# Kernel tuning notes

Hardware: AMD Instinct MI355X
Metric: run time of the kernel (lower is better)

Reference implementation:

```python
import jax, jax.numpy as jnp
import numpy as np

N = 131072      # points (rays x samples chunk)
E = 8           # spatial sub-networks (centroids)
DIN = 90        # encoded pos+dir features fed to sub-NeRFs (xyz_real=True -> x[:, 3:])
H = 256         # sub-NeRF hidden width
DOUT = 4        # rgb + sigma
MARGIN = 2.0    # boundary_margin
EPS = 1e-8


def setup_inputs() -> dict:
    key = jax.random.key(0)
    k = jax.random.split(key, 5)
    x_xyz = jax.random.uniform(k[0], (N, 3), dtype=jnp.float32)          # routing coords in [0,1)^3
    x_feat = jax.random.normal(k[1], (N, DIN), dtype=jnp.float32)        # encoded features
    x = jnp.concatenate([x_xyz, x_feat], axis=1)                         # [N, 3+DIN]
    centroids = jax.random.uniform(k[2], (E, 3), dtype=jnp.float32)
    W1 = jax.random.normal(k[3], (E, DIN, H), dtype=jnp.float32) * 0.05
    b1 = jnp.zeros((E, H), dtype=jnp.float32)
    W2 = jax.random.normal(k[4], (E, H, DOUT), dtype=jnp.float32) * 0.05
    b2 = jnp.zeros((E, DOUT), dtype=jnp.float32)
    return {"x": x, "centroids": centroids, "W1": W1, "b1": b1, "W2": W2, "b2": b2}


def reference(x, centroids, W1, b1, W2, b2):
    # --- centroid routing (torch.cdist equivalent) ---
    xyz = x[:, :3]                                                       # [N,3]
    d2 = jnp.sum((xyz[:, None, :] - centroids[None, :, :]) ** 2, axis=-1)
    dist = jnp.sqrt(jnp.maximum(d2, 0.0))                                # [N,E]
    inv = 1.0 / (dist + EPS)
    min_d = jnp.min(dist, axis=1, keepdims=True)                         # [N,1]
    inv = jnp.where(dist > MARGIN * min_d, 0.0, inv)                     # zero far experts
    weights = inv / jnp.sum(inv, axis=-1, keepdims=True)                 # [N,E], rows sum to 1

    # --- per-expert sub-NeRF MLP, weighted combine ---
    # Dense-equivalent of masked gather + weighted scatter-add: experts whose
    # weight is exactly 0 contribute nothing, matching the torch masked path.
    feat = x[:, 3:]                                                      # xyz_real=True -> drop xyz
    h = jax.nn.relu(jnp.einsum('nd,edh->enh', feat, W1) + b1[:, None, :])  # [E,N,H]
    out_e = jnp.einsum('enh,eho->eno', h, W2) + b2[:, None, :]             # [E,N,DOUT]
    return jnp.einsum('eno,ne->no', out_e, weights)                        # [N,DOUT]
```

## Files before the change

### kernel.cpp

```cpp
#include <hip/hip_runtime.h>

#define NPTS 131072
#define NE 8
#define DIN 90
#define NH 256

typedef __attribute__((ext_vector_type(8))) short bf16x8;
typedef __attribute__((ext_vector_type(4))) float f32x4;
typedef __attribute__((ext_vector_type(2))) float f32x2;
typedef __attribute__((ext_vector_type(4))) unsigned int u32x4;
typedef __attribute__((ext_vector_type(2))) unsigned int u32x2;
typedef __attribute__((ext_vector_type(4), aligned(4))) float f32x4a;
typedef __attribute__((ext_vector_type(2), aligned(4))) float f32x2a;

__device__ __forceinline__ unsigned short f2bf(float f) {
  unsigned int u = __float_as_uint(f);
  u += 0x7fffu + ((u >> 16) & 1u);
  return (unsigned short)(u >> 16);
}

#if defined(__has_builtin) && __has_builtin(__builtin_amdgcn_cvt_pk_bf16_f32)
typedef __attribute__((ext_vector_type(2))) __bf16 bf16x2;
__device__ __forceinline__ unsigned int pkbf(float f0, float f1) {
  bf16x2 r = __builtin_amdgcn_cvt_pk_bf16_f32(f0, f1);
  return __builtin_bit_cast(unsigned int, r);
}
#else
__device__ __forceinline__ unsigned int pkbf(float f0, float f1) {
  unsigned int u0 = __float_as_uint(f0) + 0x7fffu;
  unsigned int u1 = __float_as_uint(f1) + 0x7fffu;
  return __builtin_amdgcn_perm(u1, u0, 0x07060302u);
}
#endif

__device__ __forceinline__ bf16x8 cvt8(f32x4 a, f32x4 b) {
  u32x4 r;
  r[0] = pkbf(a[0], a[1]);
  r[1] = pkbf(a[2], a[3]);
  r[2] = pkbf(b[0], b[1]);
  r[3] = pkbf(b[2], b[3]);
  return __builtin_bit_cast(bf16x8, r);
}

__global__ __launch_bounds__(256) void prep(const float* __restrict__ W1,
                                            const float* __restrict__ W2,
                                            unsigned short* __restrict__ W1T,
                                            unsigned short* __restrict__ W2T) {
  const int t = threadIdx.x;
  if (blockIdx.x < 32) {
    const int e = blockIdx.x >> 2;
    const int n0 = (blockIdx.x & 3) * 64;
    __shared__ unsigned int ld[64][49];
    const int nl = t & 63;
    const int kq = t >> 6;
#pragma unroll
    for (int j = 0; j < 12; ++j) {
      const int kp2 = kq + 4 * j;
      const int k0 = 2 * kp2, k1 = k0 + 1;
      unsigned int lo = 0, hi = 0;
      if (k0 < DIN) lo = f2bf(W1[((size_t)e * DIN + k0) * NH + n0 + nl]);
      if (k1 < DIN) hi = f2bf(W1[((size_t)e * DIN + k1) * NH + n0 + nl]);
      ld[nl][kp2] = lo | (hi << 16);
    }
    __syncthreads();
    unsigned int* dst = (unsigned int*)(W1T + (size_t)(e * NH + n0) * 96);
#pragma unroll
    for (int j = 0; j < 12; ++j) {
      const int u = t + 256 * j;
      dst[u] = ld[u / 48][u % 48];
    }
  } else {
    const int e = blockIdx.x - 32;
    unsigned int* dst = (unsigned int*)W2T + (size_t)e * 2048;
    const float* src = W2 + (size_t)e * 1024;
#pragma unroll
    for (int j = 0; j < 8; ++j) {
      const int u = t + 256 * j;
      const int o = u >> 7;
      const int kp = u & 127;
      unsigned int v = 0;
      if (o < 4) {
        unsigned int lo = f2bf(src[(2 * kp) * 4 + o]);
        unsigned int hi = f2bf(src[(2 * kp + 1) * 4 + o]);
        v = lo | (hi << 16);
      }
      dst[u] = v;
    }
  }
}

__global__ __launch_bounds__(256, 3) void meganerf_main(
    const float* __restrict__ x, const float* __restrict__ cent,
    const float* __restrict__ b1, const float* __restrict__ b2,
    const unsigned short* __restrict__ W1T, const unsigned short* __restrict__ W2T,
    float* __restrict__ out) {
  __shared__ unsigned short sH[4 * 2048];
  __shared__ float sW[NE][64];
  __shared__ float sB2[64][4];
  __shared__ float sB1[NE * NH];

  const int t    = threadIdx.x;
  const int lane = t & 63;
  const int wid  = t >> 6;
  const int l15  = lane & 15;
  const int l4   = lane >> 4;
  const int row0 = blockIdx.x * 64;
  const int gbase = wid * 2048;

#pragma unroll
  for (int j = 0; j < 2; ++j)
    *(f32x4*)&sB1[t * 4 + j * 1024] = *(const f32x4a*)&b1[t * 4 + j * 1024];

  bf16x8 bfr[4][3];
#pragma unroll
  for (int nf = 0; nf < 4; ++nf) {
    const float* gr = x + (size_t)(row0 + 16 * nf + l15) * 93 + 3;
    f32x4 v0, v1;
    v0 = *(const f32x4a*)(gr + 8 * l4);
    v1 = *(const f32x4a*)(gr + 8 * l4 + 4);
    bfr[nf][0] = cvt8(v0, v1);
    v0 = *(const f32x4a*)(gr + 32 + 8 * l4);
    v1 = *(const f32x4a*)(gr + 36 + 8 * l4);
    bfr[nf][1] = cvt8(v0, v1);
    if (l4 < 3) {
      v0 = *(const f32x4a*)(gr + 64 + 8 * l4);
      v1 = *(const f32x4a*)(gr + 68 + 8 * l4);
    } else {
      f32x2 tl = *(const f32x2a*)(gr + 88);
      v0[0] = tl[0]; v0[1] = tl[1]; v0[2] = 0.f; v0[3] = 0.f;
      v1[0] = 0.f; v1[1] = 0.f; v1[2] = 0.f; v1[3] = 0.f;
    }
    bfr[nf][2] = cvt8(v0, v1);
  }

  if (t < 64) {
    const float* gx = x + (size_t)(row0 + t) * 93;
    float px = gx[0], py = gx[1], pz = gx[2];
    float dist[NE], inv[NE];
    float mind = 3.4e38f;
#pragma unroll
    for (int e = 0; e < NE; ++e) {
      float dx = px - cent[e * 3 + 0];
      float dy = py - cent[e * 3 + 1];
      float dz = pz - cent[e * 3 + 2];
      float d2 = dx * dx + dy * dy + dz * dz;
      float d = sqrtf(fmaxf(d2, 0.f));
      dist[e] = d;
      inv[e] = 1.f / (d + 1e-8f);
      mind = fminf(mind, d);
    }
    float s = 0.f;
#pragma unroll
    for (int e = 0; e < NE; ++e) {
      if (dist[e] > 2.0f * mind) inv[e] = 0.f;
      s += inv[e];
    }
    float rs = 1.f / s;
    float bb[4] = {0.f, 0.f, 0.f, 0.f};
#pragma unroll
    for (int e = 0; e < NE; ++e) {
      float w = inv[e] * rs;
      sW[e][t] = w;
#pragma unroll
      for (int o = 0; o < 4; ++o) bb[o] += w * b2[e * 4 + o];
    }
#pragma unroll
    for (int o = 0; o < 4; ++o) sB2[t][o] = bb[o];
  }
  __syncthreads();

  bf16x8 w1buf[2][6];
  bf16x8 bwbuf[2];
  float wv[4];

  auto loadW1 = [&](int idx, int buf) {
    const int e = idx >> 1, c = idx & 1;
    const unsigned short* p =
        W1T + (size_t)(e * NH + 128 * c + 32 * wid + l15) * 96 + 8 * l4;
#pragma unroll
    for (int mf = 0; mf < 2; ++mf)
#pragma unroll
      for (int ks = 0; ks < 3; ++ks)
        w1buf[buf][mf * 3 + ks] = *(const bf16x8*)(p + mf * (16 * 96) + 32 * ks);
  };
  auto loadBW = [&](int idx, int buf) {
    const int e = idx >> 1, c = idx & 1;
    bwbuf[buf] = *(const bf16x8*)(W2T + (size_t)(e * 16 + l15) * NH +
                                  128 * c + 32 * wid + 8 * l4);
  };

  loadBW(0, 0);
  loadW1(0, 0);

  f32x4 facc[4] = {{0.f, 0.f, 0.f, 0.f}, {0.f, 0.f, 0.f, 0.f},
                   {0.f, 0.f, 0.f, 0.f}, {0.f, 0.f, 0.f, 0.f}};

#pragma unroll 2
  for (int i = 0; i < 16; ++i) {
    const int e = i >> 1, c = i & 1, cur = i & 1, nxt = cur ^ 1;
    const int colbase = 128 * c + 32 * wid;

    f32x4 b1v0 = *(const f32x4*)&sB1[e * NH + colbase + 4 * l4];
    f32x4 b1v1 = *(const f32x4*)&sB1[e * NH + colbase + 16 + 4 * l4];
    if (c == 0) {
#pragma unroll
      for (int nf = 0; nf < 4; ++nf) wv[nf] = sW[e][16 * nf + l15];
    }

    const int ip = (i + 1) & 15;
    loadBW(ip, nxt);
    loadW1(ip, nxt);

#pragma unroll
    for (int mf = 0; mf < 2; ++mf) {
      const f32x4 b1v = (mf == 0) ? b1v0 : b1v1;
      f32x4 acc[4];
      __builtin_amdgcn_s_setprio(1);
#pragma unroll
      for (int nf = 0; nf < 4; ++nf)
        acc[nf] = __builtin_amdgcn_mfma_f32_16x16x32_bf16(
            w1buf[cur][mf * 3 + 0], bfr[nf][0], b1v, 0, 0, 0);
#pragma unroll
      for (int ks = 1; ks < 3; ++ks)
#pragma unroll
        for (int nf = 0; nf < 4; ++nf)
          acc[nf] = __builtin_amdgcn_mfma_f32_16x16x32_bf16(
              w1buf[cur][mf * 3 + ks], bfr[nf][ks], acc[nf], 0, 0, 0);
      __builtin_amdgcn_s_setprio(0);

#pragma unroll
      for (int nf = 0; nf < 4; ++nf) {
        const float w = wv[nf];
        f32x4 a = acc[nf];
        f32x2 p0, p1;
        p0[0] = a[0]; p0[1] = a[1];
        p1[0] = a[2]; p1[1] = a[3];
        const f32x2 z = {0.f, 0.f};
        p0 = __builtin_elementwise_max(p0, z) * w;
        p1 = __builtin_elementwise_max(p1, z) * w;
        u32x2 pk;
        pk[0] = pkbf(p0[0], p0[1]);
        pk[1] = pkbf(p1[0], p1[1]);
        *(u32x2*)&sH[gbase + (nf * 64 + (l15 + 16 * (2 * mf + (l4 >> 1)))) * 8 +
                     4 * (l4 & 1)] = pk;
      }
    }

    __builtin_amdgcn_s_setprio(1);
#pragma unroll
    for (int rf = 0; rf < 4; ++rf) {
      bf16x8 ah = *(const bf16x8*)&sH[gbase + (rf * 64 + lane) * 8];
      facc[rf] = __builtin_amdgcn_mfma_f32_16x16x32_bf16(ah, bwbuf[cur], facc[rf], 0, 0, 0);
    }
    __builtin_amdgcn_s_setprio(0);
  }

  __syncthreads();
  float* sOutP = (float*)sH;
  if (l15 < 4) {
#pragma unroll
    for (int rf = 0; rf < 4; ++rf)
#pragma unroll
      for (int r = 0; r < 4; ++r)
        sOutP[(wid * 64 + 16 * rf + 4 * l4 + r) * 4 + l15] = facc[rf][r];
  }
  __syncthreads();
  {
    const int row = t >> 2, o = t & 3;
    float v = sB2[row][o] + sOutP[(0 * 64 + row) * 4 + o] + sOutP[(1 * 64 + row) * 4 + o] +
              sOutP[(2 * 64 + row) * 4 + o] + sOutP[(3 * 64 + row) * 4 + o];
    out[row0 * 4 + t] = v;
  }
}

extern "C" void kernel_launch(void* const* d_in, const int* in_sizes, int n_in,
                              void* d_out, int out_size, void* d_ws, size_t ws_size,
                              hipStream_t stream) {
  const float* x    = (const float*)d_in[0];
  const float* cent = (const float*)d_in[1];
  const float* W1   = (const float*)d_in[2];
  const float* b1   = (const float*)d_in[3];
  const float* W2   = (const float*)d_in[4];
  const float* b2   = (const float*)d_in[5];
  float* out = (float*)d_out;

  unsigned short* W1T = (unsigned short*)d_ws;
  unsigned short* W2T = W1T + NE * NH * 96;

  prep<<<40, 256, 0, stream>>>(W1, W2, W1T, W2T);
  meganerf_main<<<NPTS / 64, 256, 0, stream>>>(x, cent, b1, b2, W1T, W2T, out);
}
```

Measured before the change: 163.5 us.

## Stage features in LDS and cut register pressure to raise occupancy

The bf16 input features, previously held in registers by every wave (12 bf16x8 per lane), are now converted once and stored in shared memory, with each wave loading its own 16 rows. Each MFMA step reads them back from LDS. The W1 double buffer is trimmed so only the first half of the next tile is prefetched, and the second half plus the W2 fragment are loaded within the current step. Launch bounds move from 3 to 4 blocks per CU. The aim is more resident waves to hide latency, paid for with extra LDS reads per step and less prefetch distance on weights.

```diff
diff --git a/kernel.cpp b/kernel.cpp
--- a/kernel.cpp
+++ b/kernel.cpp
@@ -89,12 +89,110 @@
   }
 }
 
-__global__ __launch_bounds__(256, 3) void meganerf_main(
+#define UNRL _Pragma("unroll")
+
+#define FEAT(KS, NF) \
+  (*(const bf16x8*)&sFeat[(((KS)*4 + l4) * 64 + 16 * (NF) + l15) * 8])
+
+#define MF(W_, F_, C_) __builtin_amdgcn_mfma_f32_16x16x32_bf16(W_, F_, C_, 0, 0, 0)
+
+#define LOADW1MF0(E_, C_, D0, D1, D2)                                           \
+  do {                                                                          \
+    const unsigned short* _p =                                                  \
+        W1T + (size_t)((E_) * NH + 128 * (C_) + 32 * wid + l15) * 96 + 8 * l4;  \
+    D0 = *(const bf16x8*)(_p);                                                  \
+    D1 = *(const bf16x8*)(_p + 32);                                             \
+    D2 = *(const bf16x8*)(_p + 64);                                             \
+  } while (0)
+
+#define LOADW1MF1(E_, C_)                                                       \
+  do {                                                                          \
+    const unsigned short* _p = W1T +                                            \
+        (size_t)((E_) * NH + 128 * (C_) + 32 * wid + 16 + l15) * 96 + 8 * l4;   \
+    w1m1_0 = *(const bf16x8*)(_p);                                              \
+    w1m1_1 = *(const bf16x8*)(_p + 32);                                         \
+    w1m1_2 = *(const bf16x8*)(_p + 64);                                         \
+  } while (0)
+
+#define LOADBW(E_, C_)                                                          \
+  do {                                                                          \
+    bw = *(const bf16x8*)(W2T + (size_t)((E_) * 16 + l15) * NH + 128 * (C_) +   \
+                          32 * wid + 8 * l4);                                   \
+  } while (0)
+
+#define EPI(MF_)                                                                \
+  UNRL for (int nf = 0; nf < 4; ++nf) {                                         \
+    const float _w = wv[nf];                                                    \
+    f32x4 _a = acc[nf];                                                         \
+    f32x2 _p0, _p1;                                                             \
+    _p0[0] = _a[0]; _p0[1] = _a[1];                                             \
+    _p1[0] = _a[2]; _p1[1] = _a[3];                                             \
+    const f32x2 _z = {0.f, 0.f};                                                \
+    _p0 = __builtin_elementwise_max(_p0, _z) * _w;                              \
+    _p1 = __builtin_elementwise_max(_p1, _z) * _w;                              \
+    u32x2 _pk;                                                                  \
+    _pk[0] = pkbf(_p0[0], _p0[1]);                                              \
+    _pk[1] = pkbf(_p1[0], _p1[1]);                                              \
+    *(u32x2*)&sH[gbase + (nf * 64 + (l15 + 16 * (2 * (MF_) + (l4 >> 1)))) * 8 + \
+                 4 * (l4 & 1)] = _pk;                                           \
+  }
+
+#define STEPD(E_, C_, LDWV_, EN_, CN_, CM0, CM1, CM2, NM0, NM1, NM2)            \
+  do {                                                                          \
+    const int _cb = 128 * (C_) + 32 * wid;                                      \
+    f32x4 _b1v0 = *(const f32x4*)&sB1[(E_) * NH + _cb + 4 * l4];                \
+    f32x4 _b1v1 = *(const f32x4*)&sB1[(E_) * NH + _cb + 16 + 4 * l4];           \
+    if (LDWV_) {                                                                \
+      UNRL for (int nf = 0; nf < 4; ++nf) wv[nf] = sW[(E_)][16 * nf + l15];     \
+    }                                                                           \
+    LOADW1MF1(E_, C_);                                                          \
+    LOADBW(E_, C_);                                                             \
+    LOADW1MF0(EN_, CN_, NM0, NM1, NM2);                                         \
+    {                                                                           \
+      f32x4 acc[4];                                                             \
+      bf16x8 _f0, _f1, _f2, _f3;                                                \
+      __builtin_amdgcn_s_setprio(1);                                            \
+      _f0 = FEAT(0, 0); _f1 = FEAT(0, 1); _f2 = FEAT(0, 2); _f3 = FEAT(0, 3);   \
+      acc[0] = MF(CM0, _f0, _b1v0); acc[1] = MF(CM0, _f1, _b1v0);               \
+      acc[2] = MF(CM0, _f2, _b1v0); acc[3] = MF(CM0, _f3, _b1v0);               \
+      _f0 = FEAT(1, 0); _f1 = FEAT(1, 1); _f2 = FEAT(1, 2); _f3 = FEAT(1, 3);   \
+      acc[0] = MF(CM1, _f0, acc[0]); acc[1] = MF(CM1, _f1, acc[1]);             \
+      acc[2] = MF(CM1, _f2, acc[2]); acc[3] = MF(CM1, _f3, acc[3]);             \
+      _f0 = FEAT(2, 0); _f1 = FEAT(2, 1); _f2 = FEAT(2, 2); _f3 = FEAT(2, 3);   \
+      acc[0] = MF(CM2, _f0, acc[0]); acc[1] = MF(CM2, _f1, acc[1]);             \
+      acc[2] = MF(CM2, _f2, acc[2]); acc[3] = MF(CM2, _f3, acc[3]);             \
+      __builtin_amdgcn_s_setprio(0);                                            \
+      EPI(0)                                                                    \
+      asm volatile("" ::: "memory");     \
+      __builtin_amdgcn_s_setprio(1);                                            \
+      _f0 = FEAT(0, 0); _f1 = FEAT(0, 1); _f2 = FEAT(0, 2); _f3 = FEAT(0, 3);   \
+      acc[0] = MF(w1m1_0, _f0, _b1v1); acc[1] = MF(w1m1_0, _f1, _b1v1);         \
+      acc[2] = MF(w1m1_0, _f2, _b1v1); acc[3] = MF(w1m1_0, _f3, _b1v1);         \
+      _f0 = FEAT(1, 0); _f1 = FEAT(1, 1); _f2 = FEAT(1, 2); _f3 = FEAT(1, 3);   \
+      acc[0] = MF(w1m1_1, _f0, acc[0]); acc[1] = MF(w1m1_1, _f1, acc[1]);       \
+      acc[2] = MF(w1m1_1, _f2, acc[2]); acc[3] = MF(w1m1_1, _f3, acc[3]);       \
+      _f0 = FEAT(2, 0); _f1 = FEAT(2, 1); _f2 = FEAT(2, 2); _f3 = FEAT(2, 3);   \
+      acc[0] = MF(w1m1_2, _f0, acc[0]); acc[1] = MF(w1m1_2, _f1, acc[1]);       \
+      acc[2] = MF(w1m1_2, _f2, acc[2]); acc[3] = MF(w1m1_2, _f3, acc[3]);       \
+      __builtin_amdgcn_s_setprio(0);                                            \
+      EPI(1)                                                                    \
+    }                                                                           \
+    __builtin_amdgcn_s_setprio(1);                                              \
+    UNRL for (int rf = 0; rf < 4; ++rf) {                                       \
+      bf16x8 _ah = *(const bf16x8*)&sH[gbase + (rf * 64 + lane) * 8];           \
+      facc[rf] = __builtin_amdgcn_mfma_f32_16x16x32_bf16(_ah, bw, facc[rf],     \
+                                                         0, 0, 0);              \
+    }                                                                           \
+    __builtin_amdgcn_s_setprio(0);                                              \
+  } while (0)
+
+__global__ __launch_bounds__(256, 4) void meganerf_main2(
     const float* __restrict__ x, const float* __restrict__ cent,
     const float* __restrict__ b1, const float* __restrict__ b2,
     const unsigned short* __restrict__ W1T, const unsigned short* __restrict__ W2T,
     float* __restrict__ out) {
   __shared__ unsigned short sH[4 * 2048];
+  __shared__ unsigned short sFeat[12 * 512];
   __shared__ float sW[NE][64];
   __shared__ float sB2[64][4];
   __shared__ float sB1[NE * NH];
@@ -111,17 +209,15 @@
   for (int j = 0; j < 2; ++j)
     *(f32x4*)&sB1[t * 4 + j * 1024] = *(const f32x4a*)&b1[t * 4 + j * 1024];
 
-  bf16x8 bfr[4][3];
-#pragma unroll
-  for (int nf = 0; nf < 4; ++nf) {
-    const float* gr = x + (size_t)(row0 + 16 * nf + l15) * 93 + 3;
+  {
+    const float* gr = x + (size_t)(row0 + 16 * wid + l15) * 93 + 3;
     f32x4 v0, v1;
     v0 = *(const f32x4a*)(gr + 8 * l4);
     v1 = *(const f32x4a*)(gr + 8 * l4 + 4);
-    bfr[nf][0] = cvt8(v0, v1);
+    *(bf16x8*)&sFeat[((0 * 4 + l4) * 64 + 16 * wid + l15) * 8] = cvt8(v0, v1);
     v0 = *(const f32x4a*)(gr + 32 + 8 * l4);
     v1 = *(const f32x4a*)(gr + 36 + 8 * l4);
-    bfr[nf][1] = cvt8(v0, v1);
+    *(bf16x8*)&sFeat[((1 * 4 + l4) * 64 + 16 * wid + l15) * 8] = cvt8(v0, v1);
     if (l4 < 3) {
       v0 = *(const f32x4a*)(gr + 64 + 8 * l4);
       v1 = *(const f32x4a*)(gr + 68 + 8 * l4);
@@ -130,11 +226,12 @@
       v0[0] = tl[0]; v0[1] = tl[1]; v0[2] = 0.f; v0[3] = 0.f;
       v1[0] = 0.f; v1[1] = 0.f; v1[2] = 0.f; v1[3] = 0.f;
     }
-    bfr[nf][2] = cvt8(v0, v1);
-  }
-
-  if (t < 64) {
-    const float* gx = x + (size_t)(row0 + t) * 93;
+    *(bf16x8*)&sFeat[((2 * 4 + l4) * 64 + 16 * wid + l15) * 8] = cvt8(v0, v1);
+  }
+
+  if (lane < 16) {
+    const int pt = 16 * wid + lane;
+    const float* gx = x + (size_t)(row0 + pt) * 93;
     float px = gx[0], py = gx[1], pz = gx[2];
     float dist[NE], inv[NE];
     float mind = 3.4e38f;
@@ -160,99 +257,29 @@
 #pragma unroll
     for (int e = 0; e < NE; ++e) {
       float w = inv[e] * rs;
-      sW[e][t] = w;
+      sW[e][pt] = w;
 #pragma unroll
       for (int o = 0; o < 4; ++o) bb[o] += w * b2[e * 4 + o];
     }
 #pragma unroll
-    for (int o = 0; o < 4; ++o) sB2[t][o] = bb[o];
+    for (int o = 0; o < 4; ++o) sB2[pt][o] = bb[o];
   }
   __syncthreads();
 
-  bf16x8 w1buf[2][6];
-  bf16x8 bwbuf[2];
+  bf16x8 w1A0, w1A1, w1A2, w1B0, w1B1, w1B2;
+  bf16x8 w1m1_0, w1m1_1, w1m1_2;
+  bf16x8 bw;
   float wv[4];
-
-  auto loadW1 = [&](int idx, int buf) {
-    const int e = idx >> 1, c = idx & 1;
-    const unsigned short* p =
-        W1T + (size_t)(e * NH + 128 * c + 32 * wid + l15) * 96 + 8 * l4;
-#pragma unroll
-    for (int mf = 0; mf < 2; ++mf)
-#pragma unroll
-      for (int ks = 0; ks < 3; ++ks)
-        w1buf[buf][mf * 3 + ks] = *(const bf16x8*)(p + mf * (16 * 96) + 32 * ks);
-  };
-  auto loadBW = [&](int idx, int buf) {
-    const int e = idx >> 1, c = idx & 1;
-    bwbuf[buf] = *(const bf16x8*)(W2T + (size_t)(e * 16 + l15) * NH +
-                                  128 * c + 32 * wid + 8 * l4);
-  };
-
-  loadBW(0, 0);
-  loadW1(0, 0);
-
   f32x4 facc[4] = {{0.f, 0.f, 0.f, 0.f}, {0.f, 0.f, 0.f, 0.f},
                    {0.f, 0.f, 0.f, 0.f}, {0.f, 0.f, 0.f, 0.f}};
 
-#pragma unroll 2
-  for (int i = 0; i < 16; ++i) {
-    const int e = i >> 1, c = i & 1, cur = i & 1, nxt = cur ^ 1;
-    const int colbase = 128 * c + 32 * wid;
-
-    f32x4 b1v0 = *(const f32x4*)&sB1[e * NH + colbase + 4 * l4];
-    f32x4 b1v1 = *(const f32x4*)&sB1[e * NH + colbase + 16 + 4 * l4];
-    if (c == 0) {
-#pragma unroll
-      for (int nf = 0; nf < 4; ++nf) wv[nf] = sW[e][16 * nf + l15];
-    }
-
-    const int ip = (i + 1) & 15;
-    loadBW(ip, nxt);
-    loadW1(ip, nxt);
-
-#pragma unroll
-    for (int mf = 0; mf < 2; ++mf) {
-      const f32x4 b1v = (mf == 0) ? b1v0 : b1v1;
-      f32x4 acc[4];
-      __builtin_amdgcn_s_setprio(1);
-#pragma unroll
-      for (int nf = 0; nf < 4; ++nf)
-        acc[nf] = __builtin_amdgcn_mfma_f32_16x16x32_bf16(
-            w1buf[cur][mf * 3 + 0], bfr[nf][0], b1v, 0, 0, 0);
-#pragma unroll
-      for (int ks = 1; ks < 3; ++ks)
-#pragma unroll
-        for (int nf = 0; nf < 4; ++nf)
-          acc[nf] = __builtin_amdgcn_mfma_f32_16x16x32_bf16(
-              w1buf[cur][mf * 3 + ks], bfr[nf][ks], acc[nf], 0, 0, 0);
-      __builtin_amdgcn_s_setprio(0);
-
-#pragma unroll
-      for (int nf = 0; nf < 4; ++nf) {
-        const float w = wv[nf];
-        f32x4 a = acc[nf];
-        f32x2 p0, p1;
-        p0[0] = a[0]; p0[1] = a[1];
-        p1[0] = a[2]; p1[1] = a[3];
-        const f32x2 z = {0.f, 0.f};
-        p0 = __builtin_elementwise_max(p0, z) * w;
-        p1 = __builtin_elementwise_max(p1, z) * w;
-        u32x2 pk;
-        pk[0] = pkbf(p0[0], p0[1]);
-        pk[1] = pkbf(p1[0], p1[1]);
-        *(u32x2*)&sH[gbase + (nf * 64 + (l15 + 16 * (2 * mf + (l4 >> 1)))) * 8 +
-                     4 * (l4 & 1)] = pk;
-      }
-    }
-
-    __builtin_amdgcn_s_setprio(1);
-#pragma unroll
-    for (int rf = 0; rf < 4; ++rf) {
-      bf16x8 ah = *(const bf16x8*)&sH[gbase + (rf * 64 + lane) * 8];
-      facc[rf] = __builtin_amdgcn_mfma_f32_16x16x32_bf16(ah, bwbuf[cur], facc[rf], 0, 0, 0);
-    }
-    __builtin_amdgcn_s_setprio(0);
+  LOADW1MF0(0, 0, w1A0, w1A1, w1A2);
+
+  for (int i = 0; i < 16; i += 2) {
+    const int e = i >> 1;
+    const int e2 = ((i + 2) & 15) >> 1;
+    STEPD(e, 0, 1, e, 1, w1A0, w1A1, w1A2, w1B0, w1B1, w1B2);
+    STEPD(e, 1, 0, e2, 0, w1B0, w1B1, w1B2, w1A0, w1A1, w1A2);
   }
 
   __syncthreads();
@@ -288,5 +315,5 @@
   unsigned short* W2T = W1T + NE * NH * 96;
 
   prep<<<40, 256, 0, stream>>>(W1, W2, W1T, W2T);
-  meganerf_main<<<NPTS / 64, 256, 0, stream>>>(x, cent, b1, b2, W1T, W2T, out);
-}
+  meganerf_main2<<<NPTS / 64, 256, 0, stream>>>(x, cent, b1, b2, W1T, W2T, out);
+}
```

Measured after the change: 183.6 us. 12.3% more time.
